# Kernel optimization log

Measured on AMD Instinct MI355X. Metric: run time of the kernel, lower is better.

Reference implementation:

```python
import jax, jax.numpy as jnp
import numpy as np

B, D, H, W = 2, 32, 192, 192
N_SIGMA = 3
K = 8  # max instance id; ids are 1..K, 0 = background
FG_W = 1.0
W_INST, W_VAR, W_SEED = 1.0, 10.0, 1.0


def _make_xyzm():
    # channel 0 = x (varies along W), 1 = y (along H), 2 = z (along D); pixel_{x,y,z}=1
    xm = jnp.broadcast_to(jnp.linspace(0.0, 1.0, W).reshape(1, 1, W), (D, H, W))
    ym = jnp.broadcast_to(jnp.linspace(0.0, 1.0, H).reshape(1, H, 1), (D, H, W))
    zm = jnp.broadcast_to(jnp.linspace(0.0, 1.0, D).reshape(D, 1, 1), (D, H, W))
    return jnp.stack([xm, ym, zm], 0)  # (3, D, H, W)


def setup_inputs() -> dict:
    key = jax.random.key(0)
    k1, k2, k3, k4 = jax.random.split(key, 4)
    prediction = jax.random.normal(k1, (B, 3 + N_SIGMA + 1, D, H, W), jnp.float32)
    instances = jax.random.randint(k2, (B, D, H, W), 0, K + 1, jnp.int32)
    labels = jax.random.randint(k3, (B, D, H, W), 0, 2, jnp.int32)
    center_images = jax.random.uniform(k4, (B, D, H, W)) < 5e-4  # sparse center flags
    return {"prediction": prediction, "xyzm": _make_xyzm(),
            "instances": instances, "labels": labels, "center_images": center_images}


def _lovasz_hinge_flat(logits, labels):
    # logits, labels: (N,) flat; labels in {0,1} float
    signs = 2.0 * labels - 1.0
    errors = 1.0 - logits * signs
    order = jnp.argsort(-errors)          # descending errors
    errors_s = errors[order]
    gt_s = labels[order]
    gts = gt_s.sum()
    inter = gts - jnp.cumsum(gt_s)
    union = gts + jnp.cumsum(1.0 - gt_s)
    jacc = 1.0 - inter / union
    grad = jnp.concatenate([jacc[:1], jacc[1:] - jacc[:-1]])
    return jnp.dot(jax.nn.relu(errors_s), jax.lax.stop_gradient(grad))


def _forward(prediction, xyzm, instances, labels, center_images):
    def per_batch(pred, inst, lab, cim):
        emb = jnp.tanh(pred[0:3]) + xyzm                      # (3,D,H,W)
        sigma = pred[3:3 + N_SIGMA]                           # (ns,D,H,W)
        seed = jax.nn.sigmoid(pred[3 + N_SIGMA])              # (D,H,W)
        ids = jnp.arange(1, K + 1)
        masks = (inst[None] == ids[:, None, None, None]).astype(pred.dtype)  # (K,D,H,W)
        counts = masks.sum(axis=(1, 2, 3))                    # (K,)
        valid = counts > 0
        safe = jnp.maximum(counts, 1.0)
        # center: single flagged center voxel if exactly one, else masked mean of coords
        mean_center = jnp.einsum('kdhw,cdhw->kc', masks, xyzm) / safe[:, None]
        cmask = masks * cim[None].astype(pred.dtype)
        cm_cnt = cmask.sum(axis=(1, 2, 3))
        cm_center = jnp.einsum('kdhw,cdhw->kc', cmask, xyzm)
        center = jnp.where((cm_cnt == 1.0)[:, None], cm_center, mean_center)  # (K,3)
        # sigma stats per instance; var term vs detached mean, expanded form
        m_sig = jnp.einsum('kdhw,cdhw->kc', masks, sigma)
        m_sig2 = jnp.einsum('kdhw,cdhw->kc', masks, sigma * sigma)
        s_mean = m_sig / safe[:, None]                        # (K,ns)
        s_sg = jax.lax.stop_gradient(s_mean)
        var_sum = m_sig2 - 2.0 * s_sg * m_sig + s_sg * s_sg * counts[:, None]
        var_k = var_sum.sum(1) / (N_SIGMA * safe)
        s_exp = jnp.exp(10.0 * s_mean)                        # (K,ns)
        # sum_c s_c*(emb_c-center_c)^2, expanded to avoid a (K,3,D,H,W) temp
        d2 = (jnp.einsum('kc,cdhw->kdhw', s_exp, emb * emb)
              - 2.0 * jnp.einsum('kc,cdhw->kdhw', s_exp * center, emb)
              + (s_exp * center * center).sum(1)[:, None, None, None])
        dist = jnp.exp(-d2)                                   # (K,D,H,W)
        inst_k = jax.vmap(_lovasz_hinge_flat)(
            (2.0 * dist - 1.0).reshape(K, -1), masks.reshape(K, -1))
        obj = jnp.maximum(valid.sum(), 1).astype(pred.dtype)
        instance_loss = jnp.where(valid, inst_k, 0.0).sum() / obj
        var_loss = jnp.where(valid, var_k, 0.0).sum() / obj
        bg = (lab == 0).astype(pred.dtype)
        seed_loss = (bg * seed * seed).sum()
        seed_loss = seed_loss + FG_W * (masks * (seed[None] - jax.lax.stop_gradient(dist)) ** 2).sum()
        seed_loss = seed_loss / (D * H * W)
        return W_INST * instance_loss + W_VAR * var_loss + W_SEED * seed_loss

    losses = jax.vmap(per_batch)(prediction, instances, labels, center_images)
    return losses.mean()


def reference(prediction, xyzm, instances, labels, center_images):
    return _forward(prediction, xyzm, instances, labels, center_images)
```

## Files before the change

### kernel.cpp

```cpp
#include <hip/hip_runtime.h>
#include <stdint.h>

typedef unsigned long long u64;
typedef unsigned int u32;

#define BN 2
#define DD 32
#define HH 192
#define WW 192
#define NV (DD*HH*WW)
#define KK 8
#define NSL 288
#define VPB 4096
#define NB 256
#define BOFF 1808
#define L2E 1.44269504f
#define SSLOT 11
#define NFRONT 16

__device__ __forceinline__ u64 fx(float v){ return (u64)(long long)llrintf(v*4294967296.0f); }
__device__ __forceinline__ float unfx(u64 v){ return (float)((double)(long long)v*(1.0/4294967296.0)); }
__device__ __forceinline__ float rcp_f(float x){ return __builtin_amdgcn_rcpf(x); }
__device__ __forceinline__ float exp2_f(float x){ return __builtin_amdgcn_exp2f(x); }
__device__ __forceinline__ float tanh_f(float x){ return 1.f - 2.f*rcp_f(1.f + exp2_f(x*(2.f*L2E))); }
__device__ __forceinline__ float sigm_f(float x){ return rcp_f(1.f + exp2_f(-x*L2E)); }
__device__ __forceinline__ float rfl(float x){ return __uint_as_float(__builtin_amdgcn_readfirstlane((int)__float_as_uint(x))); }

struct Cell { float cnt, cmc, mx, my, mz, g0, g1, g2, h, cmx, cmy, cmz; };
__device__ __forceinline__ Cell load_cell(const u64* __restrict__ ssh, int bb, int kq){
    u64 st[SSLOT];
    #pragma unroll
    for (int s = 0; s < SSLOT; s++){
        u64 a = 0ull;
        #pragma unroll
        for (int sh = 0; sh < 4; sh++)
            a += ssh[((size_t)(sh*BN + bb)*KK + kq)*SSLOT + s];
        st[s] = a;
    }
    Cell c;
    c.cnt = (float)(long long)(st[0] >> 32);
    c.cmc = (float)(u32)st[0];
    c.mx = (float)(long long)st[1] * (1.f/(WW-1));
    c.my = (float)(long long)st[2] * (1.f/(HH-1));
    c.mz = (float)(long long)st[3] * (1.f/(DD-1));
    c.g0 = (float)((double)(long long)st[4] * (1.0/4096.0));
    c.g1 = (float)((double)(long long)st[5] * (1.0/4096.0));
    c.g2 = (float)((double)(long long)st[6] * (1.0/4096.0));
    c.h  = (float)((double)(long long)st[7] * (1.0/2048.0));
    c.cmx = unfx(st[8]); c.cmy = unfx(st[9]); c.cmz = unfx(st[10]);
    return c;
}

__global__ __launch_bounds__(1024) void k_front(
        const u32* __restrict__ w, u32* __restrict__ fpart,
        u64* __restrict__ zero_base, int nzero_u64, u32* __restrict__ counter){
    int bid = blockIdx.x;
    if (bid == 0){
        for (int i = threadIdx.x; i < nzero_u64; i += 1024) zero_base[i] = 0ull;
        if (threadIdx.x == 0) *counter = 0u;
    }
    __shared__ u32 lfl;
    if (threadIdx.x == 0) lfl = 0u;
    __syncthreads();
    const int chunk = (BN*NV/4)/NFRONT;
    u32 f = 0;
    for (int i = bid*chunk + threadIdx.x; i < (bid+1)*chunk; i += 1024){
        u32 x = w[i];
        if (x == 0x3F800000u) f |= 1u;
        else if (x > 1u) f |= 2u;
        else if (x == 1u){ f |= 8u; if (i & 1) f |= 4u; }
    }
    if (f) atomicOr(&lfl, f);
    __syncthreads();
    if (threadIdx.x == 0) fpart[bid] = lfl;
}

__global__ __launch_bounds__(512, 8) void k_stats(
        const float* __restrict__ pred,
        const int* __restrict__ inst,
        const void* __restrict__ cim, const u32* __restrict__ fpart,
        u64* __restrict__ ssh){
    int sx = blockIdx.x, b = blockIdx.y;
    __shared__ u64 bins[8][4][25];
    __shared__ u64 cmb[8][KK][4];
    __shared__ int smode;
    for (int i = threadIdx.x; i < 8*4*25; i += 512) ((u64*)bins)[i] = 0ull;
    for (int i = threadIdx.x; i < 8*KK*4; i += 512) ((u64*)cmb)[i] = 0ull;
    if (threadIdx.x == 0){
        u32 fl = 0;
        #pragma unroll
        for (int i = 0; i < NFRONT; i++) fl |= fpart[i];
        smode = (fl & 1u) ? 2 : ((fl & 2u) ? 1 : ((fl & 4u) ? 0 : ((fl & 8u) ? 3 : 0)));
    }
    __syncthreads();
    int mode = smode;
    const float* pb = pred + (size_t)b*7*NV;
    const int* ib = inst + (size_t)b*NV;
    int wv = threadIdx.x >> 6, lp = threadIdx.x & 3;
    int g = sx*VPB + threadIdx.x*8;

    const float4* q0p = (const float4*)&pb[3*(size_t)NV + g];
    const float4* q1p = (const float4*)&pb[4*(size_t)NV + g];
    const float4* q2p = (const float4*)&pb[5*(size_t)NV + g];
    float4 sa0 = q0p[0], sb0 = q0p[1];
    float4 sa1 = q1p[0], sb1 = q1p[1];
    float4 sa2 = q2p[0], sb2 = q2p[1];
    const int4* qi = (const int4*)&ib[g];
    int4 i0 = qi[0], i1 = qi[1];
    int iy = g / WW;
    int ix = g - iy*WW;
    int iz = iy / HH; iy -= iz*HH;
    u64 fxm = fx(ix*(1.f/(WW-1)));
    u64 fdx = fx(1.f/(WW-1));
    u64 fym = fx(iy*(1.f/(HH-1)));
    u64 fzm = fx(iz*(1.f/(DD-1)));
    u32 cv8 = 0;
    size_t gi = (size_t)b*NV + g;
    if (mode == 0){
        int4 c0 = ((const int4*)&((const int*)cim)[gi])[0];
        int4 c1 = ((const int4*)&((const int*)cim)[gi])[1];
        cv8 = (c0.x?1u:0u)|(c0.y?2u:0u)|(c0.z?4u:0u)|(c0.w?8u:0u)
            | (c1.x?16u:0u)|(c1.y?32u:0u)|(c1.z?64u:0u)|(c1.w?128u:0u);
    } else if (mode == 1){
        u64 c = *(const u64*)&((const unsigned char*)cim)[gi];
        #pragma unroll
        for (int j = 0; j < 8; j++) if ((c >> (8*j)) & 0xFFull) cv8 |= 1u << j;
    } else if (mode == 2){
        float4 c0 = ((const float4*)&((const float*)cim)[gi])[0];
        float4 c1 = ((const float4*)&((const float*)cim)[gi])[1];
        cv8 = (c0.x!=0.f?1u:0u)|(c0.y!=0.f?2u:0u)|(c0.z!=0.f?4u:0u)|(c0.w!=0.f?8u:0u)
            | (c1.x!=0.f?16u:0u)|(c1.y!=0.f?32u:0u)|(c1.z!=0.f?64u:0u)|(c1.w!=0.f?128u:0u);
    } else {
        const int4* cc = (const int4*)&((const int*)cim)[2*gi];
        int4 c0 = cc[0], c1 = cc[1], c2 = cc[2], c3 = cc[3];
        cv8 = (c0.x?1u:0u)|(c0.z?2u:0u)|(c1.x?4u:0u)|(c1.z?8u:0u)
            | (c2.x?16u:0u)|(c2.z?32u:0u)|(c3.x?64u:0u)|(c3.z?128u:0u);
    }
    float s0a[8] = {sa0.x,sa0.y,sa0.z,sa0.w,sb0.x,sb0.y,sb0.z,sb0.w};
    float s1a[8] = {sa1.x,sa1.y,sa1.z,sa1.w,sb1.x,sb1.y,sb1.z,sb1.w};
    float s2a[8] = {sa2.x,sa2.y,sa2.z,sa2.w,sb2.x,sb2.y,sb2.z,sb2.w};
    int iva[8] = {i0.x,i0.y,i0.z,i0.w,i1.x,i1.y,i1.z,i1.w};
    #pragma unroll
    for (int j = 0; j < 8; j++){
        int iv = iva[j];
        if (iv >= 1 && iv <= KK){
            u64* bn = &bins[wv][lp][(iv-1)*3];
            u32 cv = (cv8 >> j) & 1u;
            u32 q0 = (u32)llrintf((s0a[j] + 16.f)*4096.f);
            u32 q1 = (u32)llrintf((s1a[j] + 16.f)*4096.f);
            u32 q2 = (u32)llrintf((s2a[j] + 16.f)*4096.f);
            float s2t = s0a[j]*s0a[j] + s1a[j]*s1a[j] + s2a[j]*s2a[j];
            u32 r = (u32)llrintf(fminf(s2t, 512.f)*2048.f);
            atomicAdd(&bn[0], (1ull << 44) | ((u64)(u32)(ix + j) << 24) | ((u64)(u32)iy << 4) | cv);
            atomicAdd(&bn[1], ((u64)q0 << 32) | q1);
            atomicAdd(&bn[2], ((u64)q2 << 32) | r);
            if (cv){
                u64* cb = &cmb[wv][iv-1][0];
                atomicAdd(&cb[0], fxm + (u64)j*fdx);
                atomicAdd(&cb[1], fym);
                atomicAdd(&cb[2], fzm);
            }
        }
    }
    __syncthreads();
    int t = threadIdx.x;
    u64* cell0 = &ssh[((size_t)((sx&3)*BN + b))*KK*SSLOT];
    if (t < KK){
        int k = t;
        u64 sA = 0ull, sB = 0ull, sC = 0ull;
        #pragma unroll
        for (int r2 = 0; r2 < 32; r2++){
            const u64* bn = &bins[r2>>2][r2&3][k*3];
            sA += bn[0]; sB += bn[1]; sC += bn[2];
        }
        u64 cnt = sA >> 44;
        if (cnt){
            u64 six = (sA >> 24) & 0xFFFFFull;
            u64 siy = (sA >> 4) & 0xFFFFFull;
            u64 cm  = sA & 0xFull;
            long long bias = (long long)(cnt * 65536ull);
            long long g0 = (long long)(sB >> 32) - bias;
            long long g1 = (long long)(sB & 0xFFFFFFFFull) - bias;
            long long g2 = (long long)(sC >> 32) - bias;
            u64 h = sC & 0xFFFFFFFFull;
            u64* cell = cell0 + (size_t)k*SSLOT;
            atomicAdd(&cell[0], (cnt << 32) | cm);
            atomicAdd(&cell[1], six);
            atomicAdd(&cell[2], siy);
            atomicAdd(&cell[3], cnt*(u64)iz);
            atomicAdd(&cell[4], (u64)g0);
            atomicAdd(&cell[5], (u64)g1);
            atomicAdd(&cell[6], (u64)g2);
            atomicAdd(&cell[7], h);
        }
    }
    if (t < KK*3){
        int k = t / 3, s = t - k*3;
        u64 acc = 0ull;
        #pragma unroll
        for (int w = 0; w < 8; w++) acc += cmb[w][k][s];
        if (acc) atomicAdd(&cell0[(size_t)k*SSLOT + 8 + s], acc);
    }
}

__global__ __launch_bounds__(512, 4) void k_hist(
        const u64* __restrict__ ssh, const float* __restrict__ pred,
        const int* __restrict__ inst, const int* __restrict__ lab,
        u32* __restrict__ hs, u64* __restrict__ bgsh){
    __shared__ u32 lh[KK*2*NB];
    __shared__ u64 fgfx, bgfx;
    __shared__ float dv[KK*6];
    int sx = blockIdx.x, b = blockIdx.y;
    if (threadIdx.x == 0){ fgfx = 0ull; bgfx = 0ull; }
    for (int i = threadIdx.x; i < KK*2*NB; i += 512) lh[i] = 0u;
    if (threadIdx.x < KK){
        int kq = threadIdx.x;
        Cell c = load_cell(ssh, b, kq);
        float safe = fmaxf(c.cnt, 1.f);
        float isafe = 1.f/safe;
        float c0 = (c.cmc == 1.f) ? c.cmx : c.mx*isafe;
        float c1 = (c.cmc == 1.f) ? c.cmy : c.my*isafe;
        float c2 = (c.cmc == 1.f) ? c.cmz : c.mz*isafe;
        dv[kq*6+0] = expf(10.f*c.g0*isafe)*L2E;
        dv[kq*6+1] = expf(10.f*c.g1*isafe)*L2E;
        dv[kq*6+2] = expf(10.f*c.g2*isafe)*L2E;
        dv[kq*6+3] = c0; dv[kq*6+4] = c1; dv[kq*6+5] = c2;
    }
    __syncthreads();
    float ax[KK], ay[KK], az[KK], cx[KK], cy[KK], cz[KK];
    #pragma unroll
    for (int k = 0; k < KK; k++){
        ax[k]=rfl(dv[k*6+0]); ay[k]=rfl(dv[k*6+1]); az[k]=rfl(dv[k*6+2]);
        cx[k]=rfl(dv[k*6+3]); cy[k]=rfl(dv[k*6+4]); cz[k]=rfl(dv[k*6+5]);
    }
    const float* pb = pred + (size_t)b*7*NV;
    const int* ib = inst + (size_t)b*NV;
    const int* lb = lab + (size_t)b*NV;
    int g = sx*VPB + threadIdx.x*8;
    const float4* q0 = (const float4*)&pb[g];
    const float4* q1 = (const float4*)&pb[(size_t)NV + g];
    const float4* q2 = (const float4*)&pb[2*(size_t)NV + g];
    const float4* q6 = (const float4*)&pb[6*(size_t)NV + g];
    float4 a0 = q0[0], b0 = q0[1];
    float4 a1 = q1[0], b1 = q1[1];
    float4 a2 = q2[0], b2 = q2[1];
    float4 a6 = q6[0], b6 = q6[1];
    const int4* qi = (const int4*)&ib[g];
    int4 i0 = qi[0], i1 = qi[1];
    const int4* ql = (const int4*)&lb[g];
    int4 l0 = ql[0], l1 = ql[1];
    int iy = g / WW;
    int ix = g - iy*WW;
    int iz = iy / HH; iy -= iz*HH;
    float xm = ix*(1.f/(WW-1)), ym = iy*(1.f/(HH-1)), zm = iz*(1.f/(DD-1));
    float p0a[8] = {a0.x,a0.y,a0.z,a0.w,b0.x,b0.y,b0.z,b0.w};
    float p1a[8] = {a1.x,a1.y,a1.z,a1.w,b1.x,b1.y,b1.z,b1.w};
    float p2a[8] = {a2.x,a2.y,a2.z,a2.w,b2.x,b2.y,b2.z,b2.w};
    float p6a[8] = {a6.x,a6.y,a6.z,a6.w,b6.x,b6.y,b6.z,b6.w};
    int iva[8] = {i0.x,i0.y,i0.z,i0.w,i1.x,i1.y,i1.z,i1.w};
    int lba[8] = {l0.x,l0.y,l0.z,l0.w,l1.x,l1.y,l1.z,l1.w};
    float e0[8], e1[8], e2[8], sd[8];
    float bgacc = 0.f;
    #pragma unroll
    for (int j = 0; j < 8; j++){
        e0[j] = tanh_f(p0a[j]) + xm + j*(1.f/(WW-1));
        e1[j] = tanh_f(p1a[j]) + ym;
        e2[j] = tanh_f(p2a[j]) + zm;
        sd[j] = sigm_f(p6a[j]);
        if (lba[j] == 0) bgacc += sd[j]*sd[j];
    }
    float fgacc = 0.f;
    #pragma unroll
    for (int k = 0; k < KK; k++){
        #pragma unroll
        for (int j = 0; j < 8; j++){
            float d0 = e0[j] - cx[k], d1 = e1[j] - cy[k], dz = e2[j] - cz[k];
            float d2 = ax[k]*d0*d0;
            d2 = fmaf(ay[k]*d1, d1, d2);
            d2 = fmaf(az[k]*dz, dz, d2);
            float dist = exp2_f(-d2);
            if (iva[j] == k + 1){
                float e = fmaf(-2.f, dist, 2.f);
                int bu = (int)(__float_as_uint(e) >> 19) - BOFF;
                bu = bu < 0 ? 0 : (bu > NB-1 ? NB-1 : bu);
                atomicAdd(&lh[k*512 + bu], 1u);
                fgacc += (sd[j] - dist)*(sd[j] - dist);
            } else {
                int bu = (int)(__float_as_uint(dist) >> 19) - (BOFF - 16);
                bu = bu < 0 ? 0 : (bu > NB-1 ? NB-1 : bu);
                atomicAdd(&lh[k*512 + NB + bu], 1u);
            }
        }
    }
    #pragma unroll
    for (int off = 32; off > 0; off >>= 1){
        fgacc += __shfl_down(fgacc, off);
        bgacc += __shfl_down(bgacc, off);
    }
    if ((threadIdx.x & 63) == 0){
        if (fgacc != 0.f) atomicAdd(&fgfx, fx(fgacc));
        if (bgacc != 0.f) atomicAdd(&bgfx, fx(bgacc));
    }
    __syncthreads();
    if (threadIdx.x == 0){
        if (bgfx) atomicAdd(&bgsh[(size_t)b*8 + (sx&7)], bgfx);
        if (fgfx) atomicAdd(&bgsh[(size_t)(2+b)*8 + (sx&7)], fgfx);
    }
    u32* out = hs + ((size_t)b*NSL + sx)*(KK*NB);
    for (int i = threadIdx.x; i < KK*NB; i += 512){
        int k = i >> 8, bu = i & 255;
        out[i] = (lh[k*512 + bu] << 16) | lh[k*512 + NB + bu];
    }
}

__global__ __launch_bounds__(1024) void k_lovasz(
        const u32* __restrict__ hs, const u64* __restrict__ ssh,
        float* __restrict__ lov, const u64* __restrict__ bgsh,
        u32* __restrict__ counter, float* __restrict__ out){
    int bk = blockIdx.x, b = bk >> 3, k = bk & 7;
    int t = threadIdx.x;
    __shared__ float s_cnt[16], s_vrk[16], s_val[16];
    if (t < 16){
        Cell c = load_cell(ssh, t >> 3, t & 7);
        float safe = fmaxf(c.cnt, 1.f);
        float isafe = 1.f/safe;
        float sm0 = c.g0*isafe, sm1 = c.g1*isafe, sm2 = c.g2*isafe;
        float vs = c.h - 2.f*(sm0*c.g0 + sm1*c.g1 + sm2*c.g2)
                 + (sm0*sm0 + sm1*sm1 + sm2*sm2)*c.cnt;
        s_vrk[t] = vs*isafe*(1.f/3.f);
        s_val[t] = c.cnt > 0.f ? 1.f : 0.f;
        s_cnt[t] = c.cnt;
    }
    __syncthreads();
    float gts = s_cnt[bk];
    float obj = fmaxf(s_val[b*8+0]+s_val[b*8+1]+s_val[b*8+2]+s_val[b*8+3]
                     +s_val[b*8+4]+s_val[b*8+5]+s_val[b*8+6]+s_val[b*8+7], 1.f);
    float coef = s_val[bk]/obj;
    float lv = 0.f;
    __shared__ u64 part[4][NB];
    __shared__ u64 wsum[4];
    __shared__ float racc[NB];
    if (gts >= 0.5f){
        int bu = (NB - 1) - (t & 255);
        int sg = t >> 8;
        u32 np = 0, nn = 0;
        const u32* base = hs + (size_t)b*NSL*(KK*NB) + k*NB + bu;
        for (int s = sg; s < NSL; s += 4){
            u32 h = base[(size_t)s*(KK*NB)];
            np += h >> 16; nn += h & 0xFFFFu;
        }
        part[sg][t & 255] = ((u64)np << 32) | nn;
        __syncthreads();
        u64 pack = 0ull, inc = 0ull;
        if (t < NB){
            pack = part[0][t] + part[1][t] + part[2][t] + part[3][t];
            int lane = t & 63;
            inc = pack;
            #pragma unroll
            for (int off = 1; off < 64; off <<= 1){
                u64 n = __shfl_up(inc, off);
                if (lane >= off) inc += n;
            }
            if (lane == 63) wsum[t >> 6] = inc;
        }
        __syncthreads();
        if (t < 4){
            u64 x = wsum[t];
            #pragma unroll
            for (int off = 1; off < 4; off <<= 1){
                u64 n = __shfl_up(x, off);
                if (t >= off) x += n;
            }
            wsum[t] = x;
        }
        __syncthreads();
        float acc = 0.f;
        if (t < NB){
            int wid = t >> 6;
            u64 excl = inc - pack + (wid ? wsum[wid - 1] : 0ull);
            u32 np2 = (u32)(pack >> 32), nn2 = (u32)pack;
            if (np2 | nn2){
                int bu2 = (NB - 1) - t;
                float Pe = (float)(u32)(excl >> 32), Qe = (float)(u32)excl;
                float Pi = Pe + (float)np2, Qi = Qe + (float)nn2;
                float je = 1.f - (gts - Pe)/(gts + Qe);
                float ji = 1.f - (gts - Pi)/(gts + Qi);
                u32 bits = ((u32)(bu2 + BOFF) << 19) | (1u << 18);
                if (bits > 0x40000000u) bits = 0x40000000u;
                acc = __uint_as_float(bits) * (ji - je);
            }
            racc[t] = acc;
        }
        __syncthreads();
        for (int off = 128; off > 0; off >>= 1){
            if (t < off) racc[t] += racc[t + off];
            __syncthreads();
        }
        lv = coef * racc[0];
    }
    if (t == 0){
        __hip_atomic_store(&lov[bk], lv, __ATOMIC_RELEASE, __HIP_MEMORY_SCOPE_AGENT);
        u32 ticket = __hip_atomic_fetch_add(counter, 1u, __ATOMIC_ACQ_REL, __HIP_MEMORY_SCOPE_AGENT);
        if (ticket == 15u){
            float tot = 0.f;
            for (int i = 0; i < 16; i++)
                tot += __hip_atomic_load(&lov[i], __ATOMIC_ACQUIRE, __HIP_MEMORY_SCOPE_AGENT);
            for (int b2 = 0; b2 < BN; b2++){
                float objb = fmaxf(s_val[b2*8+0]+s_val[b2*8+1]+s_val[b2*8+2]+s_val[b2*8+3]
                                  +s_val[b2*8+4]+s_val[b2*8+5]+s_val[b2*8+6]+s_val[b2*8+7], 1.f);
                float vp = 0.f;
                for (int kq = 0; kq < 8; kq++) vp += s_val[b2*8+kq]*s_vrk[b2*8+kq];
                float bg = 0.f, fg = 0.f;
                for (int sh = 0; sh < 8; sh++){
                    bg += unfx(bgsh[(size_t)b2*8 + sh]);
                    fg += unfx(bgsh[(size_t)(2+b2)*8 + sh]);
                }
                tot += 10.f*vp/objb + (bg + fg)*(1.f/(float)NV);
            }
            out[0] = tot * 0.5f;
        }
    }
}

extern "C" void kernel_launch(void* const* d_in, const int* in_sizes, int n_in,
                              void* d_out, int out_size, void* d_ws, size_t ws_size,
                              hipStream_t stream){
    const float* pred = (const float*)d_in[0];
    const int*   inst = (const int*)d_in[2];
    const int*   lab  = (const int*)d_in[3];
    const void*  cim  = d_in[4];

    char* ws = (char*)d_ws;
    size_t off = 0;
    u32* hs = (u32*)(ws + off);        off += (size_t)BN*NSL*KK*NB*4;
    size_t zero0 = off;
    u64* ssh = (u64*)(ws + off);       off += (size_t)4*BN*KK*SSLOT*8;
    u64* bgsh = (u64*)(ws + off);      off += (size_t)4*8*8;
    size_t zero_u64 = (off - zero0)/8;
    float* lov = (float*)(ws + off);   off += 16*4;
    u32* counter = (u32*)(ws + off);   off += 4;
    u32* fpart = (u32*)(ws + off);     off += NFRONT*4;

    k_front<<<dim3(NFRONT), dim3(1024), 0, stream>>>((const u32*)cim, fpart,
                                                     (u64*)(ws + zero0), (int)zero_u64, counter);
    k_stats<<<dim3(NSL, BN), dim3(512), 0, stream>>>(pred, inst, cim, fpart, ssh);
    k_hist<<<dim3(NSL, BN), dim3(512), 0, stream>>>(ssh, pred, inst, lab, hs, bgsh);
    k_lovasz<<<16, 1024, 0, stream>>>(hs, ssh, lov, bgsh, counter, (float*)d_out);
}
```

Baseline: 70.66 us.

## Fuse four kernels into one cooperative persistent kernel with grid syncs

Measured after the change: 187.5 us. +165.3%, slower.

```diff
diff --git a/kernel.cpp b/kernel.cpp
--- a/kernel.cpp
+++ b/kernel.cpp
@@ -1,5 +1,8 @@
 #include <hip/hip_runtime.h>
+#include <hip/hip_cooperative_groups.h>
 #include <stdint.h>
+
+namespace cg = cooperative_groups;
 
 typedef unsigned long long u64;
 typedef unsigned int u32;
@@ -16,7 +19,8 @@
 #define BOFF 1808
 #define L2E 1.44269504f
 #define SSLOT 11
-#define NFRONT 16
+#define NBLK 288
+#define SMU64 2112
 
 __device__ __forceinline__ u64 fx(float v){ return (u64)(long long)llrintf(v*4294967296.0f); }
 __device__ __forceinline__ float unfx(u64 v){ return (float)((double)(long long)v*(1.0/4294967296.0)); }
@@ -51,53 +55,51 @@
     return c;
 }
 
-__global__ __launch_bounds__(1024) void k_front(
-        const u32* __restrict__ w, u32* __restrict__ fpart,
-        u64* __restrict__ zero_base, int nzero_u64, u32* __restrict__ counter){
-    int bid = blockIdx.x;
+__device__ __forceinline__ void do_front(int bid, int t, const u32* __restrict__ w,
+        u32* __restrict__ fpart, u64* __restrict__ zero_base, int nzero_u64,
+        u32* __restrict__ counter, u32* __restrict__ sfl){
     if (bid == 0){
-        for (int i = threadIdx.x; i < nzero_u64; i += 1024) zero_base[i] = 0ull;
-        if (threadIdx.x == 0) *counter = 0u;
-    }
-    __shared__ u32 lfl;
-    if (threadIdx.x == 0) lfl = 0u;
-    __syncthreads();
-    const int chunk = (BN*NV/4)/NFRONT;
+        for (int i = t; i < nzero_u64; i += 512) zero_base[i] = 0ull;
+        if (t == 0) *counter = 0u;
+    }
+    if (t == 0) *sfl = 0u;
+    __syncthreads();
+    const int chunk = (BN*NV/4)/NBLK;
     u32 f = 0;
-    for (int i = bid*chunk + threadIdx.x; i < (bid+1)*chunk; i += 1024){
+    for (int i = bid*chunk + t; i < (bid+1)*chunk; i += 512){
         u32 x = w[i];
         if (x == 0x3F800000u) f |= 1u;
         else if (x > 1u) f |= 2u;
         else if (x == 1u){ f |= 8u; if (i & 1) f |= 4u; }
     }
-    if (f) atomicOr(&lfl, f);
-    __syncthreads();
-    if (threadIdx.x == 0) fpart[bid] = lfl;
-}
-
-__global__ __launch_bounds__(512, 8) void k_stats(
-        const float* __restrict__ pred,
-        const int* __restrict__ inst,
-        const void* __restrict__ cim, const u32* __restrict__ fpart,
-        u64* __restrict__ ssh){
-    int sx = blockIdx.x, b = blockIdx.y;
-    __shared__ u64 bins[8][4][25];
-    __shared__ u64 cmb[8][KK][4];
-    __shared__ int smode;
-    for (int i = threadIdx.x; i < 8*4*25; i += 512) ((u64*)bins)[i] = 0ull;
-    for (int i = threadIdx.x; i < 8*KK*4; i += 512) ((u64*)cmb)[i] = 0ull;
-    if (threadIdx.x == 0){
-        u32 fl = 0;
-        #pragma unroll
-        for (int i = 0; i < NFRONT; i++) fl |= fpart[i];
-        smode = (fl & 1u) ? 2 : ((fl & 2u) ? 1 : ((fl & 4u) ? 0 : ((fl & 8u) ? 3 : 0)));
-    }
-    __syncthreads();
-    int mode = smode;
+    if (f) atomicOr(sfl, f);
+    __syncthreads();
+    if (t == 0) fpart[bid] = *sfl;
+}
+
+__device__ __forceinline__ int decode_mode(int t, const u32* __restrict__ fpart, u32* __restrict__ sfl){
+    if (t == 0) *sfl = 0u;
+    __syncthreads();
+    u32 fo = 0;
+    for (int i = t; i < NBLK; i += 512) fo |= fpart[i];
+    if (fo) atomicOr(sfl, fo);
+    __syncthreads();
+    u32 fl = *sfl;
+    __syncthreads();
+    return (fl & 1u) ? 2 : ((fl & 2u) ? 1 : ((fl & 4u) ? 0 : ((fl & 8u) ? 3 : 0)));
+}
+
+__device__ __forceinline__ void do_stats_tile(int sx, int b, int mode, int t,
+        const float* __restrict__ pred, const int* __restrict__ inst,
+        const void* __restrict__ cim, u64* __restrict__ ssh, u64* __restrict__ sm8){
+    u64 (*bins)[4][25] = (u64(*)[4][25])sm8;
+    u64 (*cmb)[KK][4]  = (u64(*)[KK][4])(sm8 + 800);
+    for (int i = t; i < 800 + 256; i += 512) sm8[i] = 0ull;
+    __syncthreads();
     const float* pb = pred + (size_t)b*7*NV;
     const int* ib = inst + (size_t)b*NV;
-    int wv = threadIdx.x >> 6, lp = threadIdx.x & 3;
-    int g = sx*VPB + threadIdx.x*8;
+    int wv = t >> 6, lp = t & 3;
+    int g = sx*VPB + t*8;
 
     const float4* q0p = (const float4*)&pb[3*(size_t)NV + g];
     const float4* q1p = (const float4*)&pb[4*(size_t)NV + g];
@@ -163,7 +165,6 @@
         }
     }
     __syncthreads();
-    int t = threadIdx.x;
     u64* cell0 = &ssh[((size_t)((sx&3)*BN + b))*KK*SSLOT];
     if (t < KK){
         int k = t;
@@ -201,20 +202,21 @@
         for (int w = 0; w < 8; w++) acc += cmb[w][k][s];
         if (acc) atomicAdd(&cell0[(size_t)k*SSLOT + 8 + s], acc);
     }
-}
-
-__global__ __launch_bounds__(512, 4) void k_hist(
+    __syncthreads();
+}
+
+__device__ __forceinline__ void do_hist_tile(int sx, int b, int t,
         const u64* __restrict__ ssh, const float* __restrict__ pred,
         const int* __restrict__ inst, const int* __restrict__ lab,
-        u32* __restrict__ hs, u64* __restrict__ bgsh){
-    __shared__ u32 lh[KK*2*NB];
-    __shared__ u64 fgfx, bgfx;
-    __shared__ float dv[KK*6];
-    int sx = blockIdx.x, b = blockIdx.y;
-    if (threadIdx.x == 0){ fgfx = 0ull; bgfx = 0ull; }
-    for (int i = threadIdx.x; i < KK*2*NB; i += 512) lh[i] = 0u;
-    if (threadIdx.x < KK){
-        int kq = threadIdx.x;
+        u32* __restrict__ hs, u64* __restrict__ bgsh, u64* __restrict__ sm8){
+    u32* lh = (u32*)sm8;
+    float* dv = (float*)(sm8 + 2048);
+    u64* fgfx = sm8 + 2080;
+    u64* bgfx = sm8 + 2081;
+    if (t == 0){ *fgfx = 0ull; *bgfx = 0ull; }
+    for (int i = t; i < KK*2*NB; i += 512) lh[i] = 0u;
+    if (t < KK){
+        int kq = t;
         Cell c = load_cell(ssh, b, kq);
         float safe = fmaxf(c.cnt, 1.f);
         float isafe = 1.f/safe;
@@ -236,7 +238,7 @@
     const float* pb = pred + (size_t)b*7*NV;
     const int* ib = inst + (size_t)b*NV;
     const int* lb = lab + (size_t)b*NV;
-    int g = sx*VPB + threadIdx.x*8;
+    int g = sx*VPB + t*8;
     const float4* q0 = (const float4*)&pb[g];
     const float4* q1 = (const float4*)&pb[(size_t)NV + g];
     const float4* q2 = (const float4*)&pb[2*(size_t)NV + g];
@@ -297,29 +299,34 @@
         fgacc += __shfl_down(fgacc, off);
         bgacc += __shfl_down(bgacc, off);
     }
-    if ((threadIdx.x & 63) == 0){
-        if (fgacc != 0.f) atomicAdd(&fgfx, fx(fgacc));
-        if (bgacc != 0.f) atomicAdd(&bgfx, fx(bgacc));
-    }
-    __syncthreads();
-    if (threadIdx.x == 0){
-        if (bgfx) atomicAdd(&bgsh[(size_t)b*8 + (sx&7)], bgfx);
-        if (fgfx) atomicAdd(&bgsh[(size_t)(2+b)*8 + (sx&7)], fgfx);
+    if ((t & 63) == 0){
+        if (fgacc != 0.f) atomicAdd(fgfx, fx(fgacc));
+        if (bgacc != 0.f) atomicAdd(bgfx, fx(bgacc));
+    }
+    __syncthreads();
+    if (t == 0){
+        if (*bgfx) atomicAdd(&bgsh[(size_t)b*8 + (sx&7)], *bgfx);
+        if (*fgfx) atomicAdd(&bgsh[(size_t)(2+b)*8 + (sx&7)], *fgfx);
     }
     u32* out = hs + ((size_t)b*NSL + sx)*(KK*NB);
-    for (int i = threadIdx.x; i < KK*NB; i += 512){
+    for (int i = t; i < KK*NB; i += 512){
         int k = i >> 8, bu = i & 255;
         out[i] = (lh[k*512 + bu] << 16) | lh[k*512 + NB + bu];
     }
-}
-
-__global__ __launch_bounds__(1024) void k_lovasz(
+    __syncthreads();
+}
+
+__device__ __forceinline__ void do_lovasz(int bk, int t,
         const u32* __restrict__ hs, const u64* __restrict__ ssh,
         float* __restrict__ lov, const u64* __restrict__ bgsh,
-        u32* __restrict__ counter, float* __restrict__ out){
-    int bk = blockIdx.x, b = bk >> 3, k = bk & 7;
-    int t = threadIdx.x;
-    __shared__ float s_cnt[16], s_vrk[16], s_val[16];
+        u32* __restrict__ counter, float* __restrict__ out, u64* __restrict__ sm8){
+    int b = bk >> 3, k = bk & 7;
+    u64 (*part)[NB] = (u64(*)[NB])sm8;
+    u64* wsum = sm8 + 512;
+    float* racc = (float*)(sm8 + 516);
+    float* s_cnt = (float*)(sm8 + 648);
+    float* s_vrk = s_cnt + 16;
+    float* s_val = s_cnt + 32;
     if (t < 16){
         Cell c = load_cell(ssh, t >> 3, t & 7);
         float safe = fmaxf(c.cnt, 1.f);
@@ -337,15 +344,12 @@
                      +s_val[b*8+4]+s_val[b*8+5]+s_val[b*8+6]+s_val[b*8+7], 1.f);
     float coef = s_val[bk]/obj;
     float lv = 0.f;
-    __shared__ u64 part[4][NB];
-    __shared__ u64 wsum[4];
-    __shared__ float racc[NB];
     if (gts >= 0.5f){
         int bu = (NB - 1) - (t & 255);
         int sg = t >> 8;
         u32 np = 0, nn = 0;
         const u32* base = hs + (size_t)b*NSL*(KK*NB) + k*NB + bu;
-        for (int s = sg; s < NSL; s += 4){
+        for (int s = sg; s < NSL; s += 2){
             u32 h = base[(size_t)s*(KK*NB)];
             np += h >> 16; nn += h & 0xFFFFu;
         }
@@ -353,7 +357,7 @@
         __syncthreads();
         u64 pack = 0ull, inc = 0ull;
         if (t < NB){
-            pack = part[0][t] + part[1][t] + part[2][t] + part[3][t];
+            pack = part[0][t] + part[1][t];
             int lane = t & 63;
             inc = pack;
             #pragma unroll
@@ -422,6 +426,61 @@
     }
 }
 
+__global__ __launch_bounds__(512, 4) void k_mega(
+        const float* __restrict__ pred, const int* __restrict__ inst,
+        const int* __restrict__ lab, const void* __restrict__ cim,
+        u64* __restrict__ ssh, u64* __restrict__ bgsh, u32* __restrict__ fpart,
+        u32* __restrict__ hs, float* __restrict__ lov, u32* __restrict__ counter,
+        float* __restrict__ out, int nzero_u64){
+    cg::grid_group grid = cg::this_grid();
+    __shared__ u64 sm8[SMU64];
+    __shared__ u32 sfl;
+    int bid = blockIdx.x, t = threadIdx.x;
+    do_front(bid, t, (const u32*)cim, fpart, ssh, nzero_u64, counter, &sfl);
+    grid.sync();
+    int mode = decode_mode(t, fpart, &sfl);
+    do_stats_tile(bid, 0, mode, t, pred, inst, cim, ssh, sm8);
+    do_stats_tile(bid, 1, mode, t, pred, inst, cim, ssh, sm8);
+    grid.sync();
+    do_hist_tile(bid, 0, t, ssh, pred, inst, lab, hs, bgsh, sm8);
+    do_hist_tile(bid, 1, t, ssh, pred, inst, lab, hs, bgsh, sm8);
+    grid.sync();
+    if (bid < 16) do_lovasz(bid, t, hs, ssh, lov, bgsh, counter, out, sm8);
+}
+
+__global__ __launch_bounds__(512) void k_front(
+        const u32* __restrict__ w, u32* __restrict__ fpart,
+        u64* __restrict__ zero_base, int nzero_u64, u32* __restrict__ counter){
+    __shared__ u32 sfl;
+    do_front(blockIdx.x, threadIdx.x, w, fpart, zero_base, nzero_u64, counter, &sfl);
+}
+
+__global__ __launch_bounds__(512, 8) void k_stats(
+        const float* __restrict__ pred, const int* __restrict__ inst,
+        const void* __restrict__ cim, const u32* __restrict__ fpart,
+        u64* __restrict__ ssh){
+    __shared__ u64 sm8[1056];
+    __shared__ u32 sfl;
+    int mode = decode_mode(threadIdx.x, fpart, &sfl);
+    do_stats_tile(blockIdx.x, blockIdx.y, mode, threadIdx.x, pred, inst, cim, ssh, sm8);
+}
+
+__global__ __launch_bounds__(512, 4) void k_hist(
+        const u64* __restrict__ ssh, const float* __restrict__ pred,
+        const int* __restrict__ inst, const int* __restrict__ lab,
+        u32* __restrict__ hs, u64* __restrict__ bgsh){
+    __shared__ u64 sm8[SMU64];
+    do_hist_tile(blockIdx.x, blockIdx.y, threadIdx.x, ssh, pred, inst, lab, hs, bgsh, sm8);
+}
+
+__global__ __launch_bounds__(512) void k_lovasz(
+        const u32* __restrict__ hs, const u64* __restrict__ ssh,
+        float* __restrict__ lov, const u64* __restrict__ bgsh,
+        u32* __restrict__ counter, float* __restrict__ out){
+    __shared__ u64 sm8[800];
+    do_lovasz(blockIdx.x, threadIdx.x, hs, ssh, lov, bgsh, counter, out, sm8);
+}
+
 extern "C" void kernel_launch(void* const* d_in, const int* in_sizes, int n_in,
                               void* d_out, int out_size, void* d_ws, size_t ws_size,
                               hipStream_t stream){
@@ -429,6 +488,7 @@
     const int*   inst = (const int*)d_in[2];
     const int*   lab  = (const int*)d_in[3];
     const void*  cim  = d_in[4];
+    float* outp = (float*)d_out;
 
     char* ws = (char*)d_ws;
     size_t off = 0;
@@ -436,14 +496,20 @@
     size_t zero0 = off;
     u64* ssh = (u64*)(ws + off);       off += (size_t)4*BN*KK*SSLOT*8;
     u64* bgsh = (u64*)(ws + off);      off += (size_t)4*8*8;
-    size_t zero_u64 = (off - zero0)/8;
+    int nzero_u64 = (int)((off - zero0)/8);
     float* lov = (float*)(ws + off);   off += 16*4;
     u32* counter = (u32*)(ws + off);   off += 4;
-    u32* fpart = (u32*)(ws + off);     off += NFRONT*4;
-
-    k_front<<<dim3(NFRONT), dim3(1024), 0, stream>>>((const u32*)cim, fpart,
-                                                     (u64*)(ws + zero0), (int)zero_u64, counter);
-    k_stats<<<dim3(NSL, BN), dim3(512), 0, stream>>>(pred, inst, cim, fpart, ssh);
-    k_hist<<<dim3(NSL, BN), dim3(512), 0, stream>>>(ssh, pred, inst, lab, hs, bgsh);
-    k_lovasz<<<16, 1024, 0, stream>>>(hs, ssh, lov, bgsh, counter, (float*)d_out);
-}
+    u32* fpart = (u32*)(ws + off);     off += NBLK*4;
+
+    void* kargs[] = {(void*)&pred, (void*)&inst, (void*)&lab, (void*)&cim,
+                     (void*)&ssh, (void*)&bgsh, (void*)&fpart, (void*)&hs,
+                     (void*)&lov, (void*)&counter, (void*)&outp, (void*)&nzero_u64};
+    hipError_t e = hipLaunchCooperativeKernel(reinterpret_cast<void*>(k_mega),
+                                              dim3(NBLK), dim3(512), kargs, 0, stream);
+    if (e != hipSuccess){
+        k_front<<<dim3(NBLK), dim3(512), 0, stream>>>((const u32*)cim, fpart, ssh, nzero_u64, counter);
+        k_stats<<<dim3(NSL, BN), dim3(512), 0, stream>>>(pred, inst, cim, fpart, ssh);
+        k_hist<<<dim3(NSL, BN), dim3(512), 0, stream>>>(ssh, pred, inst, lab, hs, bgsh);
+        k_lovasz<<<16, 512, 0, stream>>>(hs, ssh, lov, bgsh, counter, outp);
+    }
+}
```

## Spread front scan over more blocks and halve per-thread work in stats/hist

Applied to the files above, without the earlier changes.

Result: no change. 69.29 us (-1.9%).

```diff
diff --git a/kernel.cpp b/kernel.cpp
--- a/kernel.cpp
+++ b/kernel.cpp
@@ -16,7 +16,7 @@
 #define BOFF 1808
 #define L2E 1.44269504f
 #define SSLOT 11
-#define NFRONT 16
+#define NFRONT 288
 
 __device__ __forceinline__ u64 fx(float v){ return (u64)(long long)llrintf(v*4294967296.0f); }
 __device__ __forceinline__ float unfx(u64 v){ return (float)((double)(long long)v*(1.0/4294967296.0)); }
@@ -51,62 +51,64 @@
     return c;
 }
 
-__global__ __launch_bounds__(1024) void k_front(
+__global__ __launch_bounds__(512) void k_front(
         const u32* __restrict__ w, u32* __restrict__ fpart,
         u64* __restrict__ zero_base, int nzero_u64, u32* __restrict__ counter){
-    int bid = blockIdx.x;
+    int bid = blockIdx.x, t = threadIdx.x;
     if (bid == 0){
-        for (int i = threadIdx.x; i < nzero_u64; i += 1024) zero_base[i] = 0ull;
-        if (threadIdx.x == 0) *counter = 0u;
-    }
-    __shared__ u32 lfl;
-    if (threadIdx.x == 0) lfl = 0u;
+        for (int i = t; i < nzero_u64; i += 512) zero_base[i] = 0ull;
+        if (t == 0) *counter = 0u;
+    }
+    __shared__ u32 sfl;
+    if (t == 0) sfl = 0u;
     __syncthreads();
     const int chunk = (BN*NV/4)/NFRONT;
     u32 f = 0;
-    for (int i = bid*chunk + threadIdx.x; i < (bid+1)*chunk; i += 1024){
+    for (int i = bid*chunk + t; i < (bid+1)*chunk; i += 512){
         u32 x = w[i];
         if (x == 0x3F800000u) f |= 1u;
         else if (x > 1u) f |= 2u;
         else if (x == 1u){ f |= 8u; if (i & 1) f |= 4u; }
     }
-    if (f) atomicOr(&lfl, f);
-    __syncthreads();
-    if (threadIdx.x == 0) fpart[bid] = lfl;
-}
-
-__global__ __launch_bounds__(512, 8) void k_stats(
-        const float* __restrict__ pred,
-        const int* __restrict__ inst,
+    if (f) atomicOr(&sfl, f);
+    __syncthreads();
+    if (t == 0) fpart[bid] = sfl;
+}
+
+__device__ __forceinline__ int decode_mode(int t, int nthr, const u32* __restrict__ fpart,
+                                           u32* __restrict__ sfl){
+    if (t == 0) *sfl = 0u;
+    __syncthreads();
+    u32 fo = 0;
+    for (int i = t; i < NFRONT; i += nthr) fo |= fpart[i];
+    if (fo) atomicOr(sfl, fo);
+    __syncthreads();
+    u32 fl = *sfl;
+    __syncthreads();
+    return (fl & 1u) ? 2 : ((fl & 2u) ? 1 : ((fl & 4u) ? 0 : ((fl & 8u) ? 3 : 0)));
+}
+
+__global__ __launch_bounds__(1024, 8) void k_stats(
+        const float* __restrict__ pred, const int* __restrict__ inst,
         const void* __restrict__ cim, const u32* __restrict__ fpart,
         u64* __restrict__ ssh){
     int sx = blockIdx.x, b = blockIdx.y;
-    __shared__ u64 bins[8][4][25];
-    __shared__ u64 cmb[8][KK][4];
-    __shared__ int smode;
-    for (int i = threadIdx.x; i < 8*4*25; i += 512) ((u64*)bins)[i] = 0ull;
-    for (int i = threadIdx.x; i < 8*KK*4; i += 512) ((u64*)cmb)[i] = 0ull;
-    if (threadIdx.x == 0){
-        u32 fl = 0;
-        #pragma unroll
-        for (int i = 0; i < NFRONT; i++) fl |= fpart[i];
-        smode = (fl & 1u) ? 2 : ((fl & 2u) ? 1 : ((fl & 4u) ? 0 : ((fl & 8u) ? 3 : 0)));
-    }
-    __syncthreads();
-    int mode = smode;
+    __shared__ u64 bins[16][4][25];
+    __shared__ u64 cmb[16][KK][4];
+    __shared__ u32 sfl;
+    for (int i = threadIdx.x; i < 16*4*25; i += 1024) ((u64*)bins)[i] = 0ull;
+    for (int i = threadIdx.x; i < 16*KK*4; i += 1024) ((u64*)cmb)[i] = 0ull;
+    int mode = decode_mode(threadIdx.x, 1024, fpart, &sfl);
     const float* pb = pred + (size_t)b*7*NV;
     const int* ib = inst + (size_t)b*NV;
-    int wv = threadIdx.x >> 6, lp = threadIdx.x & 3;
-    int g = sx*VPB + threadIdx.x*8;
-
-    const float4* q0p = (const float4*)&pb[3*(size_t)NV + g];
-    const float4* q1p = (const float4*)&pb[4*(size_t)NV + g];
-    const float4* q2p = (const float4*)&pb[5*(size_t)NV + g];
-    float4 sa0 = q0p[0], sb0 = q0p[1];
-    float4 sa1 = q1p[0], sb1 = q1p[1];
-    float4 sa2 = q2p[0], sb2 = q2p[1];
-    const int4* qi = (const int4*)&ib[g];
-    int4 i0 = qi[0], i1 = qi[1];
+    int t = threadIdx.x;
+    int wv = t >> 6, lp = t & 3;
+    int g = sx*VPB + t*4;
+
+    float4 s0v = *(const float4*)&pb[3*(size_t)NV + g];
+    float4 s1v = *(const float4*)&pb[4*(size_t)NV + g];
+    float4 s2v = *(const float4*)&pb[5*(size_t)NV + g];
+    int4 iv4 = *(const int4*)&ib[g];
     int iy = g / WW;
     int ix = g - iy*WW;
     int iz = iy / HH; iy -= iz*HH;
@@ -114,38 +116,32 @@
     u64 fdx = fx(1.f/(WW-1));
     u64 fym = fx(iy*(1.f/(HH-1)));
     u64 fzm = fx(iz*(1.f/(DD-1)));
-    u32 cv8 = 0;
+    u32 cv4 = 0;
     size_t gi = (size_t)b*NV + g;
     if (mode == 0){
-        int4 c0 = ((const int4*)&((const int*)cim)[gi])[0];
-        int4 c1 = ((const int4*)&((const int*)cim)[gi])[1];
-        cv8 = (c0.x?1u:0u)|(c0.y?2u:0u)|(c0.z?4u:0u)|(c0.w?8u:0u)
-            | (c1.x?16u:0u)|(c1.y?32u:0u)|(c1.z?64u:0u)|(c1.w?128u:0u);
+        int4 c = *(const int4*)&((const int*)cim)[gi];
+        cv4 = (c.x?1u:0u)|(c.y?2u:0u)|(c.z?4u:0u)|(c.w?8u:0u);
     } else if (mode == 1){
-        u64 c = *(const u64*)&((const unsigned char*)cim)[gi];
-        #pragma unroll
-        for (int j = 0; j < 8; j++) if ((c >> (8*j)) & 0xFFull) cv8 |= 1u << j;
+        u32 c = *(const u32*)&((const unsigned char*)cim)[gi];
+        cv4 = ((c&0xFFu)?1u:0u)|((c&0xFF00u)?2u:0u)|((c&0xFF0000u)?4u:0u)|((c&0xFF000000u)?8u:0u);
     } else if (mode == 2){
-        float4 c0 = ((const float4*)&((const float*)cim)[gi])[0];
-        float4 c1 = ((const float4*)&((const float*)cim)[gi])[1];
-        cv8 = (c0.x!=0.f?1u:0u)|(c0.y!=0.f?2u:0u)|(c0.z!=0.f?4u:0u)|(c0.w!=0.f?8u:0u)
-            | (c1.x!=0.f?16u:0u)|(c1.y!=0.f?32u:0u)|(c1.z!=0.f?64u:0u)|(c1.w!=0.f?128u:0u);
+        float4 c = *(const float4*)&((const float*)cim)[gi];
+        cv4 = (c.x!=0.f?1u:0u)|(c.y!=0.f?2u:0u)|(c.z!=0.f?4u:0u)|(c.w!=0.f?8u:0u);
     } else {
-        const int4* cc = (const int4*)&((const int*)cim)[2*gi];
-        int4 c0 = cc[0], c1 = cc[1], c2 = cc[2], c3 = cc[3];
-        cv8 = (c0.x?1u:0u)|(c0.z?2u:0u)|(c1.x?4u:0u)|(c1.z?8u:0u)
-            | (c2.x?16u:0u)|(c2.z?32u:0u)|(c3.x?64u:0u)|(c3.z?128u:0u);
-    }
-    float s0a[8] = {sa0.x,sa0.y,sa0.z,sa0.w,sb0.x,sb0.y,sb0.z,sb0.w};
-    float s1a[8] = {sa1.x,sa1.y,sa1.z,sa1.w,sb1.x,sb1.y,sb1.z,sb1.w};
-    float s2a[8] = {sa2.x,sa2.y,sa2.z,sa2.w,sb2.x,sb2.y,sb2.z,sb2.w};
-    int iva[8] = {i0.x,i0.y,i0.z,i0.w,i1.x,i1.y,i1.z,i1.w};
-    #pragma unroll
-    for (int j = 0; j < 8; j++){
+        int4 c0 = *(const int4*)&((const int*)cim)[2*gi];
+        int4 c1 = *(const int4*)&((const int*)cim)[2*gi + 4];
+        cv4 = (c0.x?1u:0u)|(c0.z?2u:0u)|(c1.x?4u:0u)|(c1.z?8u:0u);
+    }
+    float s0a[4] = {s0v.x,s0v.y,s0v.z,s0v.w};
+    float s1a[4] = {s1v.x,s1v.y,s1v.z,s1v.w};
+    float s2a[4] = {s2v.x,s2v.y,s2v.z,s2v.w};
+    int iva[4] = {iv4.x,iv4.y,iv4.z,iv4.w};
+    #pragma unroll
+    for (int j = 0; j < 4; j++){
         int iv = iva[j];
         if (iv >= 1 && iv <= KK){
             u64* bn = &bins[wv][lp][(iv-1)*3];
-            u32 cv = (cv8 >> j) & 1u;
+            u32 cv = (cv4 >> j) & 1u;
             u32 q0 = (u32)llrintf((s0a[j] + 16.f)*4096.f);
             u32 q1 = (u32)llrintf((s1a[j] + 16.f)*4096.f);
             u32 q2 = (u32)llrintf((s2a[j] + 16.f)*4096.f);
@@ -163,13 +159,12 @@
         }
     }
     __syncthreads();
-    int t = threadIdx.x;
     u64* cell0 = &ssh[((size_t)((sx&3)*BN + b))*KK*SSLOT];
     if (t < KK){
         int k = t;
         u64 sA = 0ull, sB = 0ull, sC = 0ull;
         #pragma unroll
-        for (int r2 = 0; r2 < 32; r2++){
+        for (int r2 = 0; r2 < 64; r2++){
             const u64* bn = &bins[r2>>2][r2&3][k*3];
             sA += bn[0]; sB += bn[1]; sC += bn[2];
         }
@@ -198,12 +193,12 @@
         int k = t / 3, s = t - k*3;
         u64 acc = 0ull;
         #pragma unroll
-        for (int w = 0; w < 8; w++) acc += cmb[w][k][s];
+        for (int w = 0; w < 16; w++) acc += cmb[w][k][s];
         if (acc) atomicAdd(&cell0[(size_t)k*SSLOT + 8 + s], acc);
     }
 }
 
-__global__ __launch_bounds__(512, 4) void k_hist(
+__global__ __launch_bounds__(1024, 8) void k_hist(
         const u64* __restrict__ ssh, const float* __restrict__ pred,
         const int* __restrict__ inst, const int* __restrict__ lab,
         u32* __restrict__ hs, u64* __restrict__ bgsh){
@@ -211,10 +206,11 @@
     __shared__ u64 fgfx, bgfx;
     __shared__ float dv[KK*6];
     int sx = blockIdx.x, b = blockIdx.y;
-    if (threadIdx.x == 0){ fgfx = 0ull; bgfx = 0ull; }
-    for (int i = threadIdx.x; i < KK*2*NB; i += 512) lh[i] = 0u;
-    if (threadIdx.x < KK){
-        int kq = threadIdx.x;
+    int t = threadIdx.x;
+    if (t == 0){ fgfx = 0ull; bgfx = 0ull; }
+    for (int i = t; i < KK*2*NB; i += 1024) lh[i] = 0u;
+    if (t < KK){
+        int kq = t;
         Cell c = load_cell(ssh, b, kq);
         float safe = fmaxf(c.cnt, 1.f);
         float isafe = 1.f/safe;
@@ -236,33 +232,27 @@
     const float* pb = pred + (size_t)b*7*NV;
     const int* ib = inst + (size_t)b*NV;
     const int* lb = lab + (size_t)b*NV;
-    int g = sx*VPB + threadIdx.x*8;
-    const float4* q0 = (const float4*)&pb[g];
-    const float4* q1 = (const float4*)&pb[(size_t)NV + g];
-    const float4* q2 = (const float4*)&pb[2*(size_t)NV + g];
-    const float4* q6 = (const float4*)&pb[6*(size_t)NV + g];
-    float4 a0 = q0[0], b0 = q0[1];
-    float4 a1 = q1[0], b1 = q1[1];
-    float4 a2 = q2[0], b2 = q2[1];
-    float4 a6 = q6[0], b6 = q6[1];
-    const int4* qi = (const int4*)&ib[g];
-    int4 i0 = qi[0], i1 = qi[1];
-    const int4* ql = (const int4*)&lb[g];
-    int4 l0 = ql[0], l1 = ql[1];
+    int g = sx*VPB + t*4;
+    float4 p0 = *(const float4*)&pb[g];
+    float4 p1 = *(const float4*)&pb[(size_t)NV + g];
+    float4 p2 = *(const float4*)&pb[2*(size_t)NV + g];
+    float4 p6 = *(const float4*)&pb[6*(size_t)NV + g];
+    int4 iv4 = *(const int4*)&ib[g];
+    int4 lb4 = *(const int4*)&lb[g];
     int iy = g / WW;
     int ix = g - iy*WW;
     int iz = iy / HH; iy -= iz*HH;
     float xm = ix*(1.f/(WW-1)), ym = iy*(1.f/(HH-1)), zm = iz*(1.f/(DD-1));
-    float p0a[8] = {a0.x,a0.y,a0.z,a0.w,b0.x,b0.y,b0.z,b0.w};
-    float p1a[8] = {a1.x,a1.y,a1.z,a1.w,b1.x,b1.y,b1.z,b1.w};
-    float p2a[8] = {a2.x,a2.y,a2.z,a2.w,b2.x,b2.y,b2.z,b2.w};
-    float p6a[8] = {a6.x,a6.y,a6.z,a6.w,b6.x,b6.y,b6.z,b6.w};
-    int iva[8] = {i0.x,i0.y,i0.z,i0.w,i1.x,i1.y,i1.z,i1.w};
-    int lba[8] = {l0.x,l0.y,l0.z,l0.w,l1.x,l1.y,l1.z,l1.w};
-    float e0[8], e1[8], e2[8], sd[8];
+    float p0a[4] = {p0.x,p0.y,p0.z,p0.w};
+    float p1a[4] = {p1.x,p1.y,p1.z,p1.w};
+    float p2a[4] = {p2.x,p2.y,p2.z,p2.w};
+    float p6a[4] = {p6.x,p6.y,p6.z,p6.w};
+    int iva[4] = {iv4.x,iv4.y,iv4.z,iv4.w};
+    int lba[4] = {lb4.x,lb4.y,lb4.z,lb4.w};
+    float e0[4], e1[4], e2[4], sd[4];
     float bgacc = 0.f;
     #pragma unroll
-    for (int j = 0; j < 8; j++){
+    for (int j = 0; j < 4; j++){
         e0[j] = tanh_f(p0a[j]) + xm + j*(1.f/(WW-1));
         e1[j] = tanh_f(p1a[j]) + ym;
         e2[j] = tanh_f(p2a[j]) + zm;
@@ -273,7 +263,7 @@
     #pragma unroll
     for (int k = 0; k < KK; k++){
         #pragma unroll
-        for (int j = 0; j < 8; j++){
+        for (int j = 0; j < 4; j++){
             float d0 = e0[j] - cx[k], d1 = e1[j] - cy[k], dz = e2[j] - cz[k];
             float d2 = ax[k]*d0*d0;
             d2 = fmaf(ay[k]*d1, d1, d2);
@@ -297,17 +287,17 @@
         fgacc += __shfl_down(fgacc, off);
         bgacc += __shfl_down(bgacc, off);
     }
-    if ((threadIdx.x & 63) == 0){
+    if ((t & 63) == 0){
         if (fgacc != 0.f) atomicAdd(&fgfx, fx(fgacc));
         if (bgacc != 0.f) atomicAdd(&bgfx, fx(bgacc));
     }
     __syncthreads();
-    if (threadIdx.x == 0){
+    if (t == 0){
         if (bgfx) atomicAdd(&bgsh[(size_t)b*8 + (sx&7)], bgfx);
         if (fgfx) atomicAdd(&bgsh[(size_t)(2+b)*8 + (sx&7)], fgfx);
     }
     u32* out = hs + ((size_t)b*NSL + sx)*(KK*NB);
-    for (int i = threadIdx.x; i < KK*NB; i += 512){
+    for (int i = t; i < KK*NB; i += 1024){
         int k = i >> 8, bu = i & 255;
         out[i] = (lh[k*512 + bu] << 16) | lh[k*512 + NB + bu];
     }
@@ -436,14 +426,13 @@
     size_t zero0 = off;
     u64* ssh = (u64*)(ws + off);       off += (size_t)4*BN*KK*SSLOT*8;
     u64* bgsh = (u64*)(ws + off);      off += (size_t)4*8*8;
-    size_t zero_u64 = (off - zero0)/8;
+    int nzero_u64 = (int)((off - zero0)/8);
     float* lov = (float*)(ws + off);   off += 16*4;
     u32* counter = (u32*)(ws + off);   off += 4;
     u32* fpart = (u32*)(ws + off);     off += NFRONT*4;
 
-    k_front<<<dim3(NFRONT), dim3(1024), 0, stream>>>((const u32*)cim, fpart,
-                                                     (u64*)(ws + zero0), (int)zero_u64, counter);
-    k_stats<<<dim3(NSL, BN), dim3(512), 0, stream>>>(pred, inst, cim, fpart, ssh);
-    k_hist<<<dim3(NSL, BN), dim3(512), 0, stream>>>(ssh, pred, inst, lab, hs, bgsh);
+    k_front<<<dim3(NFRONT), dim3(512), 0, stream>>>((const u32*)cim, fpart, ssh, nzero_u64, counter);
+    k_stats<<<dim3(NSL, BN), dim3(1024), 0, stream>>>(pred, inst, cim, fpart, ssh);
+    k_hist<<<dim3(NSL, BN), dim3(1024), 0, stream>>>(ssh, pred, inst, lab, hs, bgsh);
     k_lovasz<<<16, 1024, 0, stream>>>(hs, ssh, lov, bgsh, counter, (float*)d_out);
 }
```
